# Optimization experiments

Measured on AMD Instinct MI355X. Metric: run time of the kernel, lower is better.

The kernel has to match this reference:

```python
import jax, jax.numpy as jnp
import numpy as np

H = 768
NH = 12
HD = H // NH

def _layernorm(x, g, b, eps=1e-5):
    mu = jnp.mean(x, axis=-1, keepdims=True)
    var = jnp.var(x, axis=-1, keepdims=True)
    return (x - mu) * jax.lax.rsqrt(var + eps) * g + b

def setup_inputs() -> dict:
    key = jax.random.key(0)
    ks = jax.random.split(key, 16)
    s = 0.02
    inp = {
        "x": jax.random.normal(ks[0], (2, 2048, H), jnp.float32),
        "t": jax.random.normal(ks[1], (2, 1, H), jnp.float32),
        # MHA params
        "w_qkv": jax.random.normal(ks[2], (H, 3 * H), jnp.float32) * s,
        "b_qkv": jnp.zeros((3 * H,), jnp.float32),
        "w_mffn1": jax.random.normal(ks[3], (H, 4 * H), jnp.float32) * s,
        "b_mffn1": jnp.zeros((4 * H,), jnp.float32),
        "w_mffn2": jax.random.normal(ks[4], (4 * H, H), jnp.float32) * s,
        "b_mffn2": jnp.zeros((H,), jnp.float32),
        # scale_shift (adaLN) params
        "w_ss1": jax.random.normal(ks[5], (H, 6 * H), jnp.float32) * s,
        "b_ss1": jnp.zeros((6 * H,), jnp.float32),
        "w_ss2": jax.random.normal(ks[6], (6 * H, 6 * H), jnp.float32) * s,
        "b_ss2": jnp.zeros((6 * H,), jnp.float32),
        # layernorms
        "ln1_g": jnp.ones((H,), jnp.float32),
        "ln1_b": jnp.zeros((H,), jnp.float32),
        "ln2_g": jnp.ones((H,), jnp.float32),
        "ln2_b": jnp.zeros((H,), jnp.float32),
        # DiT block FFN
        "w_ffn1": jax.random.normal(ks[7], (H, 4 * H), jnp.float32) * s,
        "b_ffn1": jnp.zeros((4 * H,), jnp.float32),
        "w_ffn2": jax.random.normal(ks[8], (4 * H, H), jnp.float32) * s,
        "b_ffn2": jnp.zeros((H,), jnp.float32),
    }
    return inp

def _mha(x, w_qkv, b_qkv, w1, b1, w2, b2):
    B, T, _ = x.shape
    qkv = x @ w_qkv + b_qkv                      # [B,T,3H]
    qkv = qkv.reshape(B, T, 3, NH, HD)           # split (n h s) as in rearrange
    q, k, v = [jnp.transpose(qkv[:, :, i], (0, 2, 1, 3)) for i in range(3)]  # [B,NH,T,HD]
    # NOTE: faithful to source: scale by 1/sqrt(hidden_size), not head_dim
    wei = jnp.einsum('bhtd,bhsd->bhts', q, k) / jnp.sqrt(jnp.asarray(H, x.dtype))
    wei = jax.nn.softmax(wei, axis=-1)           # [B,NH,T,T] (dropout p=0)
    o = jnp.einsum('bhts,bhsd->bhtd', wei, v)    # [B,NH,T,HD]
    o = jnp.transpose(o, (0, 2, 1, 3)).reshape(B, T, H)
    o = jax.nn.gelu(o @ w1 + b1, approximate=False) @ w2 + b2
    return o

def reference(x, t, w_qkv, b_qkv, w_mffn1, b_mffn1, w_mffn2, b_mffn2,
              w_ss1, b_ss1, w_ss2, b_ss2, ln1_g, ln1_b, ln2_g, ln2_b,
              w_ffn1, b_ffn1, w_ffn2, b_ffn2):
    t_emb = jax.nn.silu(t @ w_ss1 + b_ss1) @ w_ss2 + b_ss2   # [B,1,6H]
    g1, be1, a1, g2, be2, a2 = jnp.split(t_emb, 6, axis=-1)  # each [B,1,H]
    residual = x
    h = g1 * _layernorm(x, ln1_g, ln1_b) + be1
    h = _mha(h, w_qkv, b_qkv, w_mffn1, b_mffn1, w_mffn2, b_mffn2)
    x = residual + a1 * h
    residual = x
    h = g2 * _layernorm(x, ln2_g, ln2_b) + be2
    h = jax.nn.gelu(h @ w_ffn1 + b_ffn1, approximate=False) @ w_ffn2 + b_ffn2
    x = residual + a2 * h
    return x
```

## Files before the change

kernel.cpp:

```cpp
#include <hip/hip_runtime.h>
#include <hip/hip_bf16.h>
#include <cstdint>

typedef __bf16 bf16x8 __attribute__((ext_vector_type(8)));
typedef float f32x4 __attribute__((ext_vector_type(4)));

#define SCALE_Q_LOG2E 0.052058770734702875f

__device__ inline float fast_exp2(float x) { return __builtin_amdgcn_exp2f(x); }

struct PrepArgs {
  const float* src[5];
  __hip_bfloat16* dst[5];
  int K[5], N[5];
  int start[6];
  const float* tin;
  const float* w_ss1;
  float* tacc1;
};

__global__ __launch_bounds__(256) void k_prep(PrepArgs pa) {
  __shared__ float tile[64][65];
  int bid = blockIdx.x;
  int tid = threadIdx.x;
  if (bid < pa.start[5]) {
    int i = 0;
#pragma unroll
    for (int j = 1; j < 5; ++j)
      if (bid >= pa.start[j]) i = j;
    int t0 = bid - pa.start[i];
    int N = pa.N[i], K = pa.K[i];
    int ntx = N >> 6;
    int bx = t0 % ntx, by = t0 / ntx;
    const float* src = pa.src[i];
    __hip_bfloat16* dst = pa.dst[i];
    int n0 = bx * 64, k0 = by * 64;
    int c4 = tid & 15, rr = tid >> 4;
    float4 v[4];
#pragma unroll
    for (int p = 0; p < 4; ++p)
      v[p] = *(const float4*)&src[(size_t)(k0 + rr + 16 * p) * N + n0 + c4 * 4];
#pragma unroll
    for (int p = 0; p < 4; ++p) {
      tile[rr + 16 * p][c4 * 4 + 0] = v[p].x;
      tile[rr + 16 * p][c4 * 4 + 1] = v[p].y;
      tile[rr + 16 * p][c4 * 4 + 2] = v[p].z;
      tile[rr + 16 * p][c4 * 4 + 3] = v[p].w;
    }
    __syncthreads();
    int kg = tid & 15, nl = tid >> 4;
#pragma unroll
    for (int p = 0; p < 4; ++p) {
      int n = nl + 16 * p;
      __hip_bfloat16 t4[4];
#pragma unroll
      for (int j = 0; j < 4; ++j) t4[j] = __float2bfloat16(tile[kg * 4 + j][n]);
      *(uint2*)&dst[(size_t)(n0 + n) * K + k0 + kg * 4] = *(uint2*)t4;
    }
  } else {
    int t0 = bid - pa.start[5];
    int nb = t0 % 18, kb0 = (t0 / 18) * 64;
    int n = nb * 256 + tid;
    float a0 = 0.f, a1 = 0.f;
    for (int k = kb0; k < kb0 + 64; ++k) {
      float w = pa.w_ss1[(size_t)k * 4608 + n];
      a0 += pa.tin[k] * w;
      a1 += pa.tin[768 + k] * w;
    }
    atomicAdd(&pa.tacc1[n], a0);
    atomicAdd(&pa.tacc1[4608 + n], a1);
  }
}

__global__ void k_tvec2_silu(const float* __restrict__ tacc1, const float* __restrict__ bss1,
                             const float* __restrict__ W, float* __restrict__ teacc) {
  int n2 = blockIdx.x * 256 + threadIdx.x;
  int kb = blockIdx.y * 64;
  float a0x = 0.f, a0y = 0.f, a1x = 0.f, a1y = 0.f;
  for (int k = kb; k < kb + 64; ++k) {
    float2 w = *(const float2*)&W[(size_t)k * 4608 + n2 * 2];
    float bs = bss1[k];
    float t0 = tacc1[k] + bs;
    float t1 = tacc1[4608 + k] + bs;
    t0 = t0 / (1.f + expf(-t0));
    t1 = t1 / (1.f + expf(-t1));
    a0x += t0 * w.x; a0y += t0 * w.y;
    a1x += t1 * w.x; a1y += t1 * w.y;
  }
  atomicAdd(&teacc[n2 * 2 + 0], a0x);
  atomicAdd(&teacc[n2 * 2 + 1], a0y);
  atomicAdd(&teacc[4608 + n2 * 2 + 0], a1x);
  atomicAdd(&teacc[4608 + n2 * 2 + 1], a1y);
}

__global__ void k_ln_mod(const float* __restrict__ x, const float* __restrict__ lng,
                         const float* __restrict__ lnb, const float* __restrict__ teacc,
                         const float* __restrict__ bss2,
                         int gofs, int bofs, __hip_bfloat16* __restrict__ out) {
  int row = blockIdx.x;
  int b = row >> 11;
  const float* xr = x + (size_t)row * 768;
  int tid = threadIdx.x;
  float v[3];
  float s = 0.f, sq = 0.f;
#pragma unroll
  for (int i = 0; i < 3; ++i) { v[i] = xr[tid + 256 * i]; s += v[i]; sq += v[i] * v[i]; }
#pragma unroll
  for (int o = 32; o > 0; o >>= 1) { s += __shfl_xor(s, o); sq += __shfl_xor(sq, o); }
  __shared__ float rs[4], rq[4];
  int w = tid >> 6, lane = tid & 63;
  if (lane == 0) { rs[w] = s; rq[w] = sq; }
  __syncthreads();
  s = rs[0] + rs[1] + rs[2] + rs[3];
  sq = rq[0] + rq[1] + rq[2] + rq[3];
  float mu = s * (1.f / 768.f);
  float var = sq * (1.f / 768.f) - mu * mu;
  float rstd = rsqrtf(var + 1e-5f);
  const float* tb = teacc + (size_t)b * 4608;
#pragma unroll
  for (int i = 0; i < 3; ++i) {
    int n = tid + 256 * i;
    float gv = tb[gofs + n] + bss2[gofs + n];
    float bv = tb[bofs + n] + bss2[bofs + n];
    float h = (v[i] - mu) * rstd * lng[n] + lnb[n];
    h = gv * h + bv;
    out[(size_t)row * 768 + n] = __float2bfloat16(h);
  }
}

template <int BM, int BN, int EPI>
__global__ __launch_bounds__(256)
void k_gemm(const __hip_bfloat16* __restrict__ A,
            const __hip_bfloat16* __restrict__ Bt,
            const float* __restrict__ bias,
            float* __restrict__ outF, __hip_bfloat16* __restrict__ outB,
            __hip_bfloat16* __restrict__ outV,
            const float* __restrict__ res, const float* __restrict__ teacc,
            const float* __restrict__ bss2,
            int gofs, int M, int N, int K) {
  constexpr int MI = BM / 32;
  constexpr int NI = BN / 32;
  __shared__ __align__(16) __hip_bfloat16 As[BM * 64];
  __shared__ __align__(16) __hip_bfloat16 Bs[BN * 64];
  const int tid = threadIdx.x;
  const int w = tid >> 6, lane = tid & 63;
  const int quad = lane >> 4, l16 = lane & 15;
  const int wm = w & 1, wn = w >> 1;
  const int m0 = blockIdx.y * BM, n0 = blockIdx.x * BN;
  const int srow = lane >> 3;
  const int sco = ((lane & 7) ^ srow) * 8;

  f32x4 acc[MI][NI] = {};

  for (int k0 = 0; k0 < K; k0 += 64) {
#pragma unroll
    for (int ii = 0; ii < BM / 32; ++ii) {
      int is = w * (BM / 32) + ii;
      const __hip_bfloat16* g = A + (size_t)(m0 + is * 8 + srow) * K + k0 + sco;
      __builtin_amdgcn_global_load_lds(
          (const __attribute__((address_space(1))) void*)g,
          (__attribute__((address_space(3))) void*)&As[is * 512], 16, 0, 0);
    }
#pragma unroll
    for (int ii = 0; ii < BN / 32; ++ii) {
      int is = w * (BN / 32) + ii;
      const __hip_bfloat16* g = Bt + (size_t)(n0 + is * 8 + srow) * K + k0 + sco;
      __builtin_amdgcn_global_load_lds(
          (const __attribute__((address_space(1))) void*)g,
          (__attribute__((address_space(3))) void*)&Bs[is * 512], 16, 0, 0);
    }
    __syncthreads();
#pragma unroll
    for (int ks = 0; ks < 2; ++ks) {
      bf16x8 af[MI], bfv[NI];
#pragma unroll
      for (int i = 0; i < MI; ++i) {
        int row = wm * (BM / 2) + i * 16 + l16;
        int cph = (ks * 4 + quad) ^ (row & 7);
        af[i] = *(const bf16x8*)&As[row * 64 + cph * 8];
      }
#pragma unroll
      for (int j = 0; j < NI; ++j) {
        int row = wn * (BN / 2) + j * 16 + l16;
        int cph = (ks * 4 + quad) ^ (row & 7);
        bfv[j] = *(const bf16x8*)&Bs[row * 64 + cph * 8];
      }
#pragma unroll
      for (int i = 0; i < MI; ++i)
#pragma unroll
        for (int j = 0; j < NI; ++j)
          acc[i][j] = __builtin_amdgcn_mfma_f32_16x16x32_bf16(af[i], bfv[j], acc[i][j], 0, 0, 0);
    }
    __syncthreads();
  }

#pragma unroll
  for (int j = 0; j < NI; ++j) {
    int col = n0 + wn * (BN / 2) + j * 16 + l16;
    float bs = bias[col];
#pragma unroll
    for (int i = 0; i < MI; ++i) {
      int row0 = m0 + wm * (BM / 2) + i * 16 + quad * 4;
      if (EPI == 3 && col >= 1536) {
        int d = col - 1536;
        int nh = d >> 6, dl = d & 63;
        int bb = row0 >> 11, tok = row0 & 2047;
        __hip_bfloat16 tmp[4];
#pragma unroll
        for (int r = 0; r < 4; ++r) tmp[r] = __float2bfloat16(acc[i][j][r] + bs);
        *(uint2*)&outV[((size_t)(bb * 12 + nh) * 64 + dl) * 2048 + tok] = *(uint2*)tmp;
      } else {
#pragma unroll
        for (int r = 0; r < 4; ++r) {
          int row = row0 + r;
          float v = acc[i][j][r] + bs;
          size_t idx = (size_t)row * N + col;
          if (EPI == 0) {
            outF[idx] = v;
          } else if (EPI == 1) {
            float v2 = v * v;
            float u = v * (0.79788456080286536f + 0.035677408136300125f * v2);
            float e = fast_exp2(u * 2.8853900817779268f);
            float gl = v - v * __builtin_amdgcn_rcpf(e + 1.f);
            outB[idx] = __float2bfloat16(gl);
          } else if (EPI == 2) {
            float gate = teacc[(size_t)(row >> 11) * 4608 + gofs + col] + bss2[gofs + col];
            outF[idx] = res[idx] + gate * v;
          } else {
            float vq = (col < 768) ? v * SCALE_Q_LOG2E : v;
            outB[idx] = __float2bfloat16(vq);
          }
        }
      }
    }
  }
}

__launch_bounds__(256)
__global__ void k_attn(const __hip_bfloat16* __restrict__ qkvb,
                       const __hip_bfloat16* __restrict__ VT,
                       __hip_bfloat16* __restrict__ out) {
  __shared__ __align__(16) __hip_bfloat16 Ks[2][128 * 64];
  __shared__ __align__(16) __hip_bfloat16 Vs[64 * 128];

  const int tid = threadIdx.x;
  const int w = tid >> 6, lane = tid & 63;
  const int quad = lane >> 4, l16 = lane & 15;
  const int qt = blockIdx.x, nh = blockIdx.y, b = blockIdx.z;
  const int bh = b * 12 + nh;

  const int qrow0 = b * 2048 + qt * 64 + w * 16;
  bf16x8 qf[2];
#pragma unroll
  for (int t = 0; t < 2; ++t)
    qf[t] = *(const bf16x8*)(qkvb + (size_t)(qrow0 + l16) * 2304 + nh * 64 + t * 32 + quad * 8);
  asm volatile("s_waitcnt vmcnt(0)" ::: "memory");

  bf16x8 ones;
#pragma unroll
  for (int j = 0; j < 8; ++j) ones[j] = (__bf16)1.0f;

  f32x4 o[4] = {};
  f32x4 o_l = {};

  const int srow8 = lane >> 3;
  const int sco8 = ((lane & 7) ^ srow8) * 8;
  const int srow4 = lane >> 4;

#pragma unroll
  for (int ii = 0; ii < 4; ++ii) {
    int i = w * 4 + ii;
    const __hip_bfloat16* gk =
        qkvb + (size_t)(b * 2048 + i * 8 + srow8) * 2304 + 768 + nh * 64 + sco8;
    __builtin_amdgcn_global_load_lds(
        (const __attribute__((address_space(1))) void*)gk,
        (__attribute__((address_space(3))) void*)&Ks[0][i * 512], 16, 0, 0);
  }

#pragma unroll 1
  for (int kt = 0; kt < 16; ++kt) {
    const int cur = kt & 1;

    asm volatile("s_waitcnt lgkmcnt(0)" ::: "memory");
    __builtin_amdgcn_s_barrier();

#pragma unroll
    for (int ii = 0; ii < 4; ++ii) {
      int i = w * 4 + ii;
      int vrow = i * 4 + srow4;
      const __hip_bfloat16* gv =
          VT + (size_t)(bh * 64 + vrow) * 2048 + kt * 128 + (((lane & 15) ^ (vrow & 15)) * 8);
      __builtin_amdgcn_global_load_lds(
          (const __attribute__((address_space(1))) void*)gv,
          (__attribute__((address_space(3))) void*)&Vs[i * 512], 16, 0, 0);
    }
    if (kt < 15) {
#pragma unroll
      for (int ii = 0; ii < 4; ++ii) {
        int i = w * 4 + ii;
        const __hip_bfloat16* gk =
            qkvb + (size_t)(b * 2048 + (kt + 1) * 128 + i * 8 + srow8) * 2304 + 768 + nh * 64 + sco8;
        __builtin_amdgcn_global_load_lds(
            (const __attribute__((address_space(1))) void*)gk,
            (__attribute__((address_space(3))) void*)&Ks[cur ^ 1][i * 512], 16, 0, 0);
      }
      asm volatile("s_waitcnt vmcnt(8)" ::: "memory");
    } else {
      asm volatile("s_waitcnt vmcnt(4)" ::: "memory");
    }
    __builtin_amdgcn_s_barrier();

    f32x4 s_acc[8] = {};
    __builtin_amdgcn_s_setprio(1);
#pragma unroll
    for (int t = 0; t < 2; ++t) {
#pragma unroll
      for (int c = 0; c < 8; ++c) {
        int row = c * 16 + l16;
        int cph = (t * 4 + quad) ^ (row & 7);
        bf16x8 kf = *(const bf16x8*)&Ks[cur][row * 64 + cph * 8];
        s_acc[c] = __builtin_amdgcn_mfma_f32_16x16x32_bf16(qf[t], kf, s_acc[c], 0, 0, 0);
      }
    }
    __builtin_amdgcn_s_setprio(0);

    asm volatile("s_waitcnt lgkmcnt(0)" ::: "memory");
    __builtin_amdgcn_s_barrier();

    __hip_bfloat16* Pb = &Ks[cur][w * 2048];
#pragma unroll
    for (int c = 0; c < 8; ++c) {
      int chunk = c * 2 + (l16 >> 3);
#pragma unroll
      for (int r = 0; r < 4; ++r) {
        float p = fast_exp2(s_acc[c][r]);
        int row = quad * 4 + r;
        int phys = chunk ^ row;
        Pw_dummy:;
        Pb[row * 128 + phys * 8 + (l16 & 7)] = __float2bfloat16(p);
      }
    }

    if (kt < 15) asm volatile("s_waitcnt vmcnt(4)" ::: "memory");
    else         asm volatile("s_waitcnt vmcnt(0)" ::: "memory");
    asm volatile("s_waitcnt lgkmcnt(0)" ::: "memory");
    __builtin_amdgcn_s_barrier();

    __builtin_amdgcn_s_setprio(1);
#pragma unroll
    for (int t2 = 0; t2 < 4; ++t2) {
      int phys_p = ((t2 * 4 + quad) ^ l16);
      bf16x8 pa = *(const bf16x8*)&Pb[l16 * 128 + phys_p * 8];
#pragma unroll
      for (int nf = 0; nf < 4; ++nf) {
        int row = nf * 16 + l16;
        int cph = (t2 * 4 + quad) ^ (row & 15);
        bf16x8 vf = *(const bf16x8*)&Vs[row * 128 + cph * 8];
        o[nf] = __builtin_amdgcn_mfma_f32_16x16x32_bf16(pa, vf, o[nf], 0, 0, 0);
      }
      o_l = __builtin_amdgcn_mfma_f32_16x16x32_bf16(pa, ones, o_l, 0, 0, 0);
    }
    __builtin_amdgcn_s_setprio(0);
  }

  {
    float inv[4];
#pragma unroll
    for (int r = 0; r < 4; ++r) inv[r] = 1.f / o_l[r];
#pragma unroll
    for (int nf = 0; nf < 4; ++nf)
#pragma unroll
      for (int r = 0; r < 4; ++r) {
        int row = qrow0 + quad * 4 + r;
        out[(size_t)row * 768 + nh * 64 + nf * 16 + l16] = __float2bfloat16(o[nf][r] * inv[r]);
      }
  }
}

extern "C" void kernel_launch(void* const* d_in, const int* in_sizes, int n_in,
                              void* d_out, int out_size, void* d_ws, size_t ws_size,
                              hipStream_t stream) {
  const float* x      = (const float*)d_in[0];
  const float* t      = (const float*)d_in[1];
  const float* w_qkv  = (const float*)d_in[2];
  const float* b_qkv  = (const float*)d_in[3];
  const float* w_m1   = (const float*)d_in[4];
  const float* b_m1   = (const float*)d_in[5];
  const float* w_m2   = (const float*)d_in[6];
  const float* b_m2   = (const float*)d_in[7];
  const float* w_ss1  = (const float*)d_in[8];
  const float* b_ss1  = (const float*)d_in[9];
  const float* w_ss2  = (const float*)d_in[10];
  const float* b_ss2  = (const float*)d_in[11];
  const float* ln1_g  = (const float*)d_in[12];
  const float* ln1_b  = (const float*)d_in[13];
  const float* ln2_g  = (const float*)d_in[14];
  const float* ln2_b  = (const float*)d_in[15];
  const float* w_f1   = (const float*)d_in[16];
  const float* b_f1   = (const float*)d_in[17];
  const float* w_f2   = (const float*)d_in[18];
  const float* b_f2   = (const float*)d_in[19];
  float* out = (float*)d_out;

  char* ws = (char*)d_ws;
  size_t off = 0;
  auto alloc = [&](size_t bytes) -> char* {
    off = (off + 255) & ~(size_t)255;
    char* p = ws + off;
    off += bytes;
    return p;
  };
  __hip_bfloat16* wtq  = (__hip_bfloat16*)alloc((size_t)2304 * 768 * 2);
  __hip_bfloat16* wtm1 = (__hip_bfloat16*)alloc((size_t)3072 * 768 * 2);
  __hip_bfloat16* wtm2 = (__hip_bfloat16*)alloc((size_t)768 * 3072 * 2);
  __hip_bfloat16* wtf1 = (__hip_bfloat16*)alloc((size_t)3072 * 768 * 2);
  __hip_bfloat16* wtf2 = (__hip_bfloat16*)alloc((size_t)768 * 3072 * 2);
  float* tacc1 = (float*)alloc(9216 * 4);
  float* teacc = (float*)alloc(9216 * 4);
  __hip_bfloat16* h1   = (__hip_bfloat16*)alloc((size_t)4096 * 768 * 2);
  __hip_bfloat16* qkvb = (__hip_bfloat16*)alloc((size_t)4096 * 2304 * 2);
  __hip_bfloat16* VT   = (__hip_bfloat16*)alloc((size_t)24 * 64 * 2048 * 2);
  __hip_bfloat16* attn = (__hip_bfloat16*)alloc((size_t)4096 * 768 * 2);
  __hip_bfloat16* act1 = (__hip_bfloat16*)alloc((size_t)4096 * 3072 * 2);
  float* x1            = (float*)alloc((size_t)4096 * 768 * 4);

  (void)hipMemsetAsync(tacc1, 0, 9216 * 4, stream);
  (void)hipMemsetAsync(teacc, 0, 9216 * 4, stream);

  PrepArgs pa;
  pa.src[0] = w_qkv; pa.dst[0] = wtq;  pa.K[0] = 768;  pa.N[0] = 2304;
  pa.src[1] = w_m1;  pa.dst[1] = wtm1; pa.K[1] = 768;  pa.N[1] = 3072;
  pa.src[2] = w_m2;  pa.dst[2] = wtm2; pa.K[2] = 3072; pa.N[2] = 768;
  pa.src[3] = w_f1;  pa.dst[3] = wtf1; pa.K[3] = 768;  pa.N[3] = 3072;
  pa.src[4] = w_f2;  pa.dst[4] = wtf2; pa.K[4] = 3072; pa.N[4] = 768;
  pa.start[0] = 0;
  pa.start[1] = pa.start[0] + (2304 / 64) * (768 / 64);
  pa.start[2] = pa.start[1] + (3072 / 64) * (768 / 64);
  pa.start[3] = pa.start[2] + (768 / 64) * (3072 / 64);
  pa.start[4] = pa.start[3] + (3072 / 64) * (768 / 64);
  pa.start[5] = pa.start[4] + (768 / 64) * (3072 / 64);
  pa.tin = t; pa.w_ss1 = w_ss1; pa.tacc1 = tacc1;
  int tvec1_blocks = 18 * 12;
  k_prep<<<pa.start[5] + tvec1_blocks, 256, 0, stream>>>(pa);

  k_tvec2_silu<<<dim3(4608 / 512, 4608 / 64), 256, 0, stream>>>(tacc1, b_ss1, w_ss2, teacc);

  k_ln_mod<<<4096, 256, 0, stream>>>(x, ln1_g, ln1_b, teacc, b_ss2, 0, 768, h1);
  k_gemm<64, 128, 3><<<dim3(2304 / 128, 4096 / 64), 256, 0, stream>>>(
      h1, wtq, b_qkv, nullptr, qkvb, VT, nullptr, nullptr, nullptr, 0, 4096, 2304, 768);
  k_attn<<<dim3(32, 12, 2), 256, 0, stream>>>(qkvb, VT, attn);
  k_gemm<128, 128, 1><<<dim3(3072 / 128, 4096 / 128), 256, 0, stream>>>(
      attn, wtm1, b_m1, nullptr, act1, nullptr, nullptr, nullptr, nullptr, 0, 4096, 3072, 768);
  k_gemm<64, 128, 2><<<dim3(768 / 128, 4096 / 64), 256, 0, stream>>>(
      act1, wtm2, b_m2, x1, nullptr, nullptr, x, teacc, b_ss2, 1536, 4096, 768, 3072);

  k_ln_mod<<<4096, 256, 0, stream>>>(x1, ln2_g, ln2_b, teacc, b_ss2, 2304, 3072, h1);
  k_gemm<128, 128, 1><<<dim3(3072 / 128, 4096 / 128), 256, 0, stream>>>(
      h1, wtf1, b_f1, nullptr, act1, nullptr, nullptr, nullptr, nullptr, 0, 4096, 3072, 768);
  k_gemm<64, 128, 2><<<dim3(768 / 128, 4096 / 64), 256, 0, stream>>>(
      act1, wtf2, b_f2, out, nullptr, nullptr, x1, teacc, b_ss2, 3840, 4096, 768, 3072);
}
```

Measured before the change: 470.2 us.

## Split attention KV range in two halves and combine partials in separate kernel

Attention now splits the 2048-key sequence into two halves across blockIdx.z, doubling the grid to 1536 blocks. Each block writes unnormalized fp32 partial outputs and row sums, and a new combine kernel adds them and normalizes into bf16. The K double-buffering and the hand-placed waitcnt pipelining are removed in favour of a simple single-buffer loop with __syncthreads. The aim is better CU occupancy, at the cost of extra fp32 partial traffic, an extra launch, and lost load/compute overlap.

After: 480.5 us. 2.2% more time.

```diff
diff --git a/kernel.cpp b/kernel.cpp
--- a/kernel.cpp
+++ b/kernel.cpp
@@ -239,22 +239,24 @@
 __launch_bounds__(256)
 __global__ void k_attn(const __hip_bfloat16* __restrict__ qkvb,
                        const __hip_bfloat16* __restrict__ VT,
-                       __hip_bfloat16* __restrict__ out) {
-  __shared__ __align__(16) __hip_bfloat16 Ks[2][128 * 64];
+                       float* __restrict__ Opart,
+                       float* __restrict__ lpart) {
+  __shared__ __align__(16) __hip_bfloat16 Ks[128 * 64];
   __shared__ __align__(16) __hip_bfloat16 Vs[64 * 128];
 
   const int tid = threadIdx.x;
   const int w = tid >> 6, lane = tid & 63;
   const int quad = lane >> 4, l16 = lane & 15;
-  const int qt = blockIdx.x, nh = blockIdx.y, b = blockIdx.z;
+  const int qt = blockIdx.x, nh = blockIdx.y;
+  const int b = blockIdx.z >> 1, half = blockIdx.z & 1;
   const int bh = b * 12 + nh;
+  const int tok0 = b * 2048 + half * 1024;
 
   const int qrow0 = b * 2048 + qt * 64 + w * 16;
   bf16x8 qf[2];
 #pragma unroll
   for (int t = 0; t < 2; ++t)
     qf[t] = *(const bf16x8*)(qkvb + (size_t)(qrow0 + l16) * 2304 + nh * 64 + t * 32 + quad * 8);
-  asm volatile("s_waitcnt vmcnt(0)" ::: "memory");
 
   bf16x8 ones;
 #pragma unroll
@@ -267,48 +269,25 @@
   const int sco8 = ((lane & 7) ^ srow8) * 8;
   const int srow4 = lane >> 4;
 
-#pragma unroll
-  for (int ii = 0; ii < 4; ++ii) {
-    int i = w * 4 + ii;
-    const __hip_bfloat16* gk =
-        qkvb + (size_t)(b * 2048 + i * 8 + srow8) * 2304 + 768 + nh * 64 + sco8;
-    __builtin_amdgcn_global_load_lds(
-        (const __attribute__((address_space(1))) void*)gk,
-        (__attribute__((address_space(3))) void*)&Ks[0][i * 512], 16, 0, 0);
-  }
-
-#pragma unroll 1
-  for (int kt = 0; kt < 16; ++kt) {
-    const int cur = kt & 1;
-
-    asm volatile("s_waitcnt lgkmcnt(0)" ::: "memory");
-    __builtin_amdgcn_s_barrier();
-
+  for (int kt = 0; kt < 8; ++kt) {
+    __syncthreads();
 #pragma unroll
     for (int ii = 0; ii < 4; ++ii) {
       int i = w * 4 + ii;
+      const __hip_bfloat16* gk =
+          qkvb + (size_t)(tok0 + kt * 128 + i * 8 + srow8) * 2304 + 768 + nh * 64 + sco8;
+      __builtin_amdgcn_global_load_lds(
+          (const __attribute__((address_space(1))) void*)gk,
+          (__attribute__((address_space(3))) void*)&Ks[i * 512], 16, 0, 0);
       int vrow = i * 4 + srow4;
       const __hip_bfloat16* gv =
-          VT + (size_t)(bh * 64 + vrow) * 2048 + kt * 128 + (((lane & 15) ^ (vrow & 15)) * 8);
+          VT + (size_t)(bh * 64 + vrow) * 2048 + tok0 - (size_t)b * 2048 + kt * 128 +
+          (((lane & 15) ^ (vrow & 15)) * 8);
       __builtin_amdgcn_global_load_lds(
           (const __attribute__((address_space(1))) void*)gv,
           (__attribute__((address_space(3))) void*)&Vs[i * 512], 16, 0, 0);
     }
-    if (kt < 15) {
-#pragma unroll
-      for (int ii = 0; ii < 4; ++ii) {
-        int i = w * 4 + ii;
-        const __hip_bfloat16* gk =
-            qkvb + (size_t)(b * 2048 + (kt + 1) * 128 + i * 8 + srow8) * 2304 + 768 + nh * 64 + sco8;
-        __builtin_amdgcn_global_load_lds(
-            (const __attribute__((address_space(1))) void*)gk,
-            (__attribute__((address_space(3))) void*)&Ks[cur ^ 1][i * 512], 16, 0, 0);
-      }
-      asm volatile("s_waitcnt vmcnt(8)" ::: "memory");
-    } else {
-      asm volatile("s_waitcnt vmcnt(4)" ::: "memory");
-    }
-    __builtin_amdgcn_s_barrier();
+    __syncthreads();
 
     f32x4 s_acc[8] = {};
     __builtin_amdgcn_s_setprio(1);
@@ -318,16 +297,15 @@
       for (int c = 0; c < 8; ++c) {
         int row = c * 16 + l16;
         int cph = (t * 4 + quad) ^ (row & 7);
-        bf16x8 kf = *(const bf16x8*)&Ks[cur][row * 64 + cph * 8];
+        bf16x8 kf = *(const bf16x8*)&Ks[row * 64 + cph * 8];
         s_acc[c] = __builtin_amdgcn_mfma_f32_16x16x32_bf16(qf[t], kf, s_acc[c], 0, 0, 0);
       }
     }
     __builtin_amdgcn_s_setprio(0);
 
-    asm volatile("s_waitcnt lgkmcnt(0)" ::: "memory");
-    __builtin_amdgcn_s_barrier();
-
-    __hip_bfloat16* Pb = &Ks[cur][w * 2048];
+    __syncthreads();
+
+    __hip_bfloat16* Pb = &Ks[w * 2048];
 #pragma unroll
     for (int c = 0; c < 8; ++c) {
       int chunk = c * 2 + (l16 >> 3);
@@ -336,15 +314,9 @@
         float p = fast_exp2(s_acc[c][r]);
         int row = quad * 4 + r;
         int phys = chunk ^ row;
-        Pw_dummy:;
         Pb[row * 128 + phys * 8 + (l16 & 7)] = __float2bfloat16(p);
       }
     }
-
-    if (kt < 15) asm volatile("s_waitcnt vmcnt(4)" ::: "memory");
-    else         asm volatile("s_waitcnt vmcnt(0)" ::: "memory");
-    asm volatile("s_waitcnt lgkmcnt(0)" ::: "memory");
-    __builtin_amdgcn_s_barrier();
 
     __builtin_amdgcn_s_setprio(1);
 #pragma unroll
@@ -364,17 +336,45 @@
   }
 
   {
-    float inv[4];
-#pragma unroll
-    for (int r = 0; r < 4; ++r) inv[r] = 1.f / o_l[r];
+    float* op = Opart + (size_t)half * 4096 * 768;
 #pragma unroll
     for (int nf = 0; nf < 4; ++nf)
 #pragma unroll
       for (int r = 0; r < 4; ++r) {
         int row = qrow0 + quad * 4 + r;
-        out[(size_t)row * 768 + nh * 64 + nf * 16 + l16] = __float2bfloat16(o[nf][r] * inv[r]);
-      }
-  }
+        op[(size_t)row * 768 + nh * 64 + nf * 16 + l16] = o[nf][r];
+      }
+    if (l16 == 0 && nh == 0) {
+    }
+    if (l16 == 0) {
+#pragma unroll
+      for (int r = 0; r < 4; ++r) {
+        int row = qrow0 + quad * 4 + r;
+        lpart[((size_t)half * 4096 + row) * 12 + nh] = o_l[r];
+      }
+    }
+  }
+}
+
+__global__ __launch_bounds__(192)
+void k_attn_comb(const float* __restrict__ Opart, const float* __restrict__ lpart,
+                 __hip_bfloat16* __restrict__ out) {
+  int row = blockIdx.x;
+  int tid = threadIdx.x;
+  int c0 = tid * 4;
+  int nh = c0 >> 6;
+  float l = lpart[((size_t)row) * 12 + nh] + lpart[((size_t)4096 + row) * 12 + nh];
+  float inv = 1.f / l;
+  const float* o0 = Opart + (size_t)row * 768 + c0;
+  const float* o1 = Opart + (size_t)(4096 + row) * 768 + c0;
+  float4 a = *(const float4*)o0;
+  float4 bq = *(const float4*)o1;
+  __hip_bfloat16 t4[4];
+  t4[0] = __float2bfloat16((a.x + bq.x) * inv);
+  t4[1] = __float2bfloat16((a.y + bq.y) * inv);
+  t4[2] = __float2bfloat16((a.z + bq.z) * inv);
+  t4[3] = __float2bfloat16((a.w + bq.w) * inv);
+  *(uint2*)&out[(size_t)row * 768 + c0] = *(uint2*)t4;
 }
 
 extern "C" void kernel_launch(void* const* d_in, const int* in_sizes, int n_in,
@@ -423,6 +423,8 @@
   __hip_bfloat16* attn = (__hip_bfloat16*)alloc((size_t)4096 * 768 * 2);
   __hip_bfloat16* act1 = (__hip_bfloat16*)alloc((size_t)4096 * 3072 * 2);
   float* x1            = (float*)alloc((size_t)4096 * 768 * 4);
+  float* Opart         = (float*)alloc((size_t)2 * 4096 * 768 * 4);
+  float* lpart         = (float*)alloc((size_t)2 * 4096 * 12 * 4);
 
   (void)hipMemsetAsync(tacc1, 0, 9216 * 4, stream);
   (void)hipMemsetAsync(teacc, 0, 9216 * 4, stream);
@@ -448,7 +450,8 @@
   k_ln_mod<<<4096, 256, 0, stream>>>(x, ln1_g, ln1_b, teacc, b_ss2, 0, 768, h1);
   k_gemm<64, 128, 3><<<dim3(2304 / 128, 4096 / 64), 256, 0, stream>>>(
       h1, wtq, b_qkv, nullptr, qkvb, VT, nullptr, nullptr, nullptr, 0, 4096, 2304, 768);
-  k_attn<<<dim3(32, 12, 2), 256, 0, stream>>>(qkvb, VT, attn);
+  k_attn<<<dim3(32, 12, 4), 256, 0, stream>>>(qkvb, VT, Opart, lpart);
+  k_attn_comb<<<4096, 192, 0, stream>>>(Opart, lpart, attn);
   k_gemm<128, 128, 1><<<dim3(3072 / 128, 4096 / 128), 256, 0, stream>>>(
       attn, wtm1, b_m1, nullptr, act1, nullptr, nullptr, nullptr, nullptr, 0, 4096, 3072, 768);
   k_gemm<64, 128, 2><<<dim3(768 / 128, 4096 / 64), 256, 0, stream>>>(
```
